# Kernel optimization log

Measured on AMD Instinct MI355X. Metric: run time of the kernel, lower is better.

The kernel has to match this reference:

```python
import jax, jax.numpy as jnp
import numpy as np

B, C, H, W = 8, 512, 64, 64
DEPTH, HEADS = 4, 8


def setup_inputs() -> dict:
    key = jax.random.key(0)
    ks = jax.random.split(key, 7)
    s = 0.02
    return {
        "x": jax.random.normal(ks[0], (B, C, H, W), jnp.float32),
        # axial positional embeddings, emb dim at index 1: (1,C,H,1) and (1,C,1,W)
        "pos_h": jax.random.normal(ks[1], (C, H), jnp.float32) * s,
        "pos_w": jax.random.normal(ks[2], (C, W), jnp.float32) * s,
        # per layer, per axis (0=height, 1=width): q, kv, out projections
        "wq": jax.random.normal(ks[3], (DEPTH, 2, C, C), jnp.float32) * s,
        "wkv": jax.random.normal(ks[4], (DEPTH, 2, C, 2 * C), jnp.float32) * s,
        "wo": jax.random.normal(ks[5], (DEPTH, 2, C, C), jnp.float32) * s,
        "wo_b": jax.random.normal(ks[6], (DEPTH, 2, C), jnp.float32) * s,
    }


def _attn_last_axis(x, wq, wkv, wo, wo_b, heads):
    """Self-attention along the second-to-last axis. x: (..., L, C)."""
    lead = x.shape[:-2]
    L, Cd = x.shape[-2], x.shape[-1]
    e = Cd // heads
    q = x @ wq                       # (..., L, C)
    k, v = jnp.split(x @ wkv, 2, axis=-1)
    sh = lead + (L, heads, e)
    q, k, v = q.reshape(sh), k.reshape(sh), v.reshape(sh)
    dots = jnp.einsum('...ihe,...jhe->...hij', q, k) * (e ** -0.5)
    attn = jax.nn.softmax(dots, axis=-1)
    out = jnp.einsum('...hij,...jhe->...ihe', attn, v).reshape(lead + (L, heads * e))
    return out @ wo + wo_b


def reference(x, pos_h, pos_w, wq, wkv, wo, wo_b):
    # positional embedding: x + (1,C,H,1) + (1,C,1,W)
    x = x + pos_h[None, :, :, None] + pos_w[None, :, None, :]
    y = jnp.transpose(x, (0, 2, 3, 1))  # (B,H,W,C) channels-last working layout
    for l in range(DEPTH):
        # height-axis attention: (B,W,H,C), attend along H
        yh = jnp.transpose(y, (0, 2, 1, 3))
        oh = _attn_last_axis(yh, wq[l, 0], wkv[l, 0], wo[l, 0], wo_b[l, 0], HEADS)
        oh = jnp.transpose(oh, (0, 2, 1, 3))
        # width-axis attention: attend along W
        ow = _attn_last_axis(y, wq[l, 1], wkv[l, 1], wo[l, 1], wo_b[l, 1], HEADS)
        y = oh + ow  # sum_axial_out=True, no residual
    return jnp.transpose(y, (0, 3, 1, 2))  # back to (B,C,H,W)
```

## Files before the change

### kernel.cpp

```cpp
#include <hip/hip_runtime.h>
#include <stdint.h>


typedef __attribute__((ext_vector_type(8))) short bf16x8;
typedef __attribute__((ext_vector_type(4))) float f32x4;
typedef unsigned short u16;
typedef unsigned int u32;

#define MFMA16(a, b, c) __builtin_amdgcn_mfma_f32_16x16x32_bf16((a), (b), (c), 0, 0, 0)

__device__ __forceinline__ float b2f(u16 h) {
    u32 u = ((u32)h) << 16;
    float f;
    __builtin_memcpy(&f, &u, 4);
    return f;
}
__device__ __forceinline__ u16 f2b(float f) {
    u32 u;
    __builtin_memcpy(&u, &f, 4);
    u32 r = (u + 0x7fffu + ((u >> 16) & 1u)) >> 16;
    return (u16)r;
}

#define GLD_LDS16(g, l)                                                        \
    __builtin_amdgcn_global_load_lds(                                          \
        (const __attribute__((address_space(1))) void*)(g),                    \
        (__attribute__((address_space(3))) void*)(l), 16, 0, 0)

__global__ __launch_bounds__(256) void embed_kernel(
    const float* __restrict__ x, const float* __restrict__ ph,
    const float* __restrict__ pw, u16* __restrict__ y)
{
    __shared__ float tile[64][65];
    const int c0 = blockIdx.x * 64, h = blockIdx.y, b = blockIdx.z;
    const int t = threadIdx.x;
#pragma unroll
    for (int i = 0; i < 4; ++i) {
        int cl = (t >> 4) + i * 16;
        int w4 = (t & 15) * 4;
        const float* src = x + (((size_t)(b * 512 + c0 + cl)) * 64 + h) * 64 + w4;
        float4 v = *(const float4*)src;
        float p = ph[(c0 + cl) * 64 + h];
        tile[cl][w4 + 0] = v.x + p + pw[(c0 + cl) * 64 + w4 + 0];
        tile[cl][w4 + 1] = v.y + p + pw[(c0 + cl) * 64 + w4 + 1];
        tile[cl][w4 + 2] = v.z + p + pw[(c0 + cl) * 64 + w4 + 2];
        tile[cl][w4 + 3] = v.w + p + pw[(c0 + cl) * 64 + w4 + 3];
    }
    __syncthreads();
    const int wl = t >> 2, cb = (t & 3) * 16;
    bf16x8 o0, o1;
#pragma unroll
    for (int j = 0; j < 8; ++j) o0[j] = (short)f2b(tile[cb + j][wl]);
#pragma unroll
    for (int j = 0; j < 8; ++j) o1[j] = (short)f2b(tile[cb + 8 + j][wl]);
    u16* dst = y + (((size_t)(b * 64 + h) * 64 + wl) * 512 + c0 + cb);
    *(bf16x8*)dst = o0;
    *(bf16x8*)(dst + 8) = o1;
}

__global__ __launch_bounds__(256) void wtrans_kernel(
    const float* __restrict__ wq, const float* __restrict__ wkv,
    const float* __restrict__ wo, u16* __restrict__ wT)
{
    const int mid = blockIdx.z;
    const int l = mid / 6, rest = mid % 6, axis = rest / 3, which = rest % 3;
    const size_t la = (size_t)(l * 2 + axis);
    const float* src;
    int N;
    size_t doff;
    if (which == 0)      { src = wq  + la * 512 * 512;  N = 512;  doff = la * (2048 * 512); }
    else if (which == 1) { src = wkv + la * 512 * 1024; N = 1024; doff = la * (2048 * 512) + 512 * 512; }
    else                 { src = wo  + la * 512 * 512;  N = 512;  doff = la * (2048 * 512) + 512 * 512 + 1024 * 512; }
    const int n0 = blockIdx.y * 64;
    if (n0 >= N) return;
    const int k0 = blockIdx.x * 64;
    __shared__ float tile[64][65];
    const int t = threadIdx.x;
#pragma unroll
    for (int i = 0; i < 4; ++i) {
        int kl = (t >> 4) + i * 16;
        int n4 = (t & 15) * 4;
        float4 v = *(const float4*)(src + (size_t)(k0 + kl) * N + n0 + n4);
        tile[kl][n4 + 0] = v.x; tile[kl][n4 + 1] = v.y;
        tile[kl][n4 + 2] = v.z; tile[kl][n4 + 3] = v.w;
    }
    __syncthreads();
    const int nl = t >> 2, kb = (t & 3) * 16;
    bf16x8 o0, o1;
#pragma unroll
    for (int j = 0; j < 8; ++j) o0[j] = (short)f2b(tile[kb + j][nl]);
#pragma unroll
    for (int j = 0; j < 8; ++j) o1[j] = (short)f2b(tile[kb + 8 + j][nl]);
    u16* dst = wT + doff + (size_t)(n0 + nl) * 512 + k0 + kb;
    *(bf16x8*)dst = o0;
    *(bf16x8*)(dst + 8) = o1;
}

template <int MODE, int PERM>
__global__ __launch_bounds__(512, 2) void gemm256(
    const u16* __restrict__ A, int lda,
    const u16* __restrict__ Bt,
    const float* __restrict__ bias,
    u16* C, int ldc)
{
    __shared__ u16 As[2][256 * 64];
    __shared__ u16 Bs[2][256 * 64];
    const int tid = threadIdx.x, lane = tid & 63, wid = tid >> 6;
    const int wm = wid >> 2, wn = wid & 3;
    int lin = blockIdx.x + gridDim.x * blockIdx.y;
    int cpx = (gridDim.x * gridDim.y) >> 3;
    int id = (lin & 7) * cpx + (lin >> 3);
    const int n0 = (id % gridDim.x) * 256;
    const int m0 = (id / gridDim.x) * 256;
    const int rl = lane >> 3, cp = lane & 7, l16 = lane & 15, g = lane >> 4;
    const int kgrp = g << 3;

    f32x4 acc[4][8] = {};

#define STAGE(b, ks)                                                           \
    {                                                                          \
        _Pragma("unroll")                                                      \
        for (int j = 0; j < 4; ++j) {                                          \
            int grp = wid + 8 * j;                                             \
            int row = grp * 8 + rl;                                            \
            const u16* s = A + (size_t)(m0 + row) * lda + (ks) + (cp ^ (row & 7)) * 8; \
            GLD_LDS16(s, As[b] + grp * 512);                                   \
        }                                                                      \
        _Pragma("unroll")                                                      \
        for (int j = 0; j < 4; ++j) {                                          \
            int grp = wid + 8 * j;                                             \
            int row = grp * 8 + rl;                                            \
            const u16* s = Bt + (size_t)(n0 + row) * 512 + (ks) + (cp ^ (row & 7)) * 8; \
            GLD_LDS16(s, Bs[b] + grp * 512);                                   \
        }                                                                      \
    }

#define FRAG(base, row, kk)                                                    \
    (*(const bf16x8*)((const char*)(base) + (row) * 128 +                      \
                      (((kk) * 64 + g * 16) ^ (((row) & 7) << 4))))

    STAGE(0, 0);

    for (int t = 0; t < 8; ++t) {
        const int cb = t & 1;
        if (t < 7) STAGE(cb ^ 1, (t + 1) * 64);
        __builtin_amdgcn_sched_barrier(0);
        if (t < 7) { asm volatile("s_waitcnt vmcnt(8)" ::: "memory"); }
        else       { asm volatile("s_waitcnt vmcnt(0)" ::: "memory"); }
        __builtin_amdgcn_s_barrier();
        __builtin_amdgcn_sched_barrier(0);

        const u16* cA = As[cb];
        const u16* cB = Bs[cb];
        bf16x8 bl[2][2], bh[2][2], af[4][2];

#pragma unroll
        for (int nf = 0; nf < 2; ++nf)
#pragma unroll
            for (int kk = 0; kk < 2; ++kk)
                bl[nf][kk] = FRAG(cB, wn * 64 + nf * 16 + l16, kk);
#pragma unroll
        for (int mf = 0; mf < 4; ++mf)
#pragma unroll
            for (int kk = 0; kk < 2; ++kk)
                af[mf][kk] = FRAG(cA, wm * 128 + mf * 16 + l16, kk);
        __builtin_amdgcn_s_setprio(1);
#pragma unroll
        for (int kk = 0; kk < 2; ++kk)
#pragma unroll
            for (int nf = 0; nf < 2; ++nf)
#pragma unroll
                for (int mf = 0; mf < 4; ++mf)
                    acc[nf][mf] = MFMA16(bl[nf][kk], af[mf][kk], acc[nf][mf]);
        __builtin_amdgcn_s_setprio(0);

#pragma unroll
        for (int nf = 0; nf < 2; ++nf)
#pragma unroll
            for (int kk = 0; kk < 2; ++kk)
                bh[nf][kk] = FRAG(cB, wn * 64 + 32 + nf * 16 + l16, kk);
        __builtin_amdgcn_s_setprio(1);
#pragma unroll
        for (int kk = 0; kk < 2; ++kk)
#pragma unroll
            for (int nf = 0; nf < 2; ++nf)
#pragma unroll
                for (int mf = 0; mf < 4; ++mf)
                    acc[2 + nf][mf] = MFMA16(bh[nf][kk], af[mf][kk], acc[2 + nf][mf]);
        __builtin_amdgcn_s_setprio(0);

#pragma unroll
        for (int mf = 0; mf < 4; ++mf)
#pragma unroll
            for (int kk = 0; kk < 2; ++kk)
                af[mf][kk] = FRAG(cA, wm * 128 + 64 + mf * 16 + l16, kk);
        __builtin_amdgcn_s_setprio(1);
#pragma unroll
        for (int kk = 0; kk < 2; ++kk)
#pragma unroll
            for (int nf = 0; nf < 2; ++nf)
#pragma unroll
                for (int mf = 0; mf < 4; ++mf)
                    acc[2 + nf][4 + mf] = MFMA16(bh[nf][kk], af[mf][kk], acc[2 + nf][4 + mf]);
        __builtin_amdgcn_s_setprio(0);

        __builtin_amdgcn_s_setprio(1);
#pragma unroll
        for (int kk = 0; kk < 2; ++kk)
#pragma unroll
            for (int nf = 0; nf < 2; ++nf)
#pragma unroll
                for (int mf = 0; mf < 4; ++mf)
                    acc[nf][4 + mf] = MFMA16(bl[nf][kk], af[mf][kk], acc[nf][4 + mf]);
        __builtin_amdgcn_s_setprio(0);

        __builtin_amdgcn_sched_barrier(0);
        __builtin_amdgcn_s_barrier();
        __builtin_amdgcn_sched_barrier(0);
    }

    float bv[4][4];
    if (MODE >= 1) {
#pragma unroll
        for (int nf = 0; nf < 4; ++nf) {
            float4 b4 = *(const float4*)(bias + n0 + wn * 64 + nf * 16 + g * 4);
            bv[nf][0] = b4.x; bv[nf][1] = b4.y; bv[nf][2] = b4.z; bv[nf][3] = b4.w;
        }
    }
#pragma unroll
    for (int mf = 0; mf < 8; ++mf) {
        const int m = m0 + wm * 128 + mf * 16 + l16;
        const int mp = PERM ? ((m & ~4095) | ((m & 63) << 6) | ((m >> 6) & 63)) : m;
        u16* crow = C + (size_t)mp * ldc;
#pragma unroll
        for (int nf = 0; nf < 4; ++nf) {
            const int n = n0 + wn * 64 + nf * 16 + g * 4;
            u16* cptr = crow + n;
            float v0 = acc[nf][mf][0], v1 = acc[nf][mf][1];
            float v2 = acc[nf][mf][2], v3 = acc[nf][mf][3];
            if (MODE >= 1) { v0 += bv[nf][0]; v1 += bv[nf][1]; v2 += bv[nf][2]; v3 += bv[nf][3]; }
            if (MODE == 2) {
                ushort4 o = *(const ushort4*)cptr;
                v0 += b2f(o.x); v1 += b2f(o.y); v2 += b2f(o.z); v3 += b2f(o.w);
            }
            uint2 pk;
            pk.x = (u32)f2b(v0) | ((u32)f2b(v1) << 16);
            pk.y = (u32)f2b(v2) | ((u32)f2b(v3) << 16);
            *(uint2*)cptr = pk;
        }
    }
#undef STAGE
#undef FRAG
}

__global__ __launch_bounds__(256) void attn_kernel(u16* QKV)
{
    __shared__ u16 sm[4][2][64 * 64];
    const int tid = threadIdx.x, lane = tid & 63, wv = tid >> 6;
    const int unit = blockIdx.x * 4 + wv;
    const int base = (unit >> 3) * 64;
    const int hoff = (unit & 7) * 64;
    const int l16 = lane & 15, g = lane >> 4;
    const int kgrp = g << 3;
    const int rl = lane >> 3, cp = lane & 7;
    u16* Kl = (u16*)sm[wv][0];
    u16* Vt = (u16*)sm[wv][1];

#pragma unroll
    for (int i = 0; i < 8; ++i) {
        int row = i * 8 + rl;
        int clog = cp ^ (row & 7);
        const u16* src = QKV + (size_t)(base + row) * 1536 + 512 + hoff + clog * 8;
        GLD_LDS16(src, Kl + i * 8 * 64);
    }
    bf16x8 q[4][2];
#pragma unroll
    for (int i_f = 0; i_f < 4; ++i_f)
#pragma unroll
        for (int k2 = 0; k2 < 2; ++k2)
            q[i_f][k2] = *(const bf16x8*)(QKV + (size_t)(base + i_f * 16 + l16) * 1536
                                          + hoff + k2 * 32 + kgrp);
    bf16x8 vvr[8];
#pragma unroll
    for (int i = 0; i < 8; ++i)
        vvr[i] = *(const bf16x8*)(QKV + (size_t)(base + i * 8 + rl) * 1536
                                  + 1024 + hoff + cp * 8);

    asm volatile("s_waitcnt vmcnt(0)" ::: "memory");
    __builtin_amdgcn_sched_barrier(0);

    f32x4 st[4][4] = {};
#pragma unroll
    for (int k2 = 0; k2 < 2; ++k2) {
        bf16x8 kf[4];
        const int kb = (k2 * 32 + kgrp) * 2;
#pragma unroll
        for (int j_f = 0; j_f < 4; ++j_f) {
            int row = j_f * 16 + l16;
            kf[j_f] = *(const bf16x8*)((const char*)Kl + row * 128 + (kb ^ ((row & 7) << 4)));
        }
#pragma unroll
        for (int i_f = 0; i_f < 4; ++i_f)
#pragma unroll
            for (int j_f = 0; j_f < 4; ++j_f)
                st[i_f][j_f] = MFMA16(kf[j_f], q[i_f][k2], st[i_f][j_f]);
    }

#pragma unroll
    for (int i = 0; i < 8; ++i) {
        int j2 = i * 16 + rl * 2;
#pragma unroll
        for (int t = 0; t < 8; ++t) {
            int e = cp * 8 + t;
            int addr = e * 128 + (j2 ^ (((t ^ cp) & 7) << 4));
            *(u16*)((char*)Vt + addr) = (u16)vvr[i][t];
        }
    }

#pragma unroll
    for (int i_f = 0; i_f < 4; ++i_f) {
        const int irow = i_f * 16 + l16;
        float ev[4][4];
        float mx = -1e30f;
#pragma unroll
        for (int j_f = 0; j_f < 4; ++j_f)
#pragma unroll
            for (int r = 0; r < 4; ++r) {
                float v = st[i_f][j_f][r] * 0.125f;
                ev[j_f][r] = v;
                mx = fmaxf(mx, v);
            }
        mx = fmaxf(mx, __shfl_xor(mx, 16, 64));
        mx = fmaxf(mx, __shfl_xor(mx, 32, 64));
        float sum = 0.f;
#pragma unroll
        for (int j_f = 0; j_f < 4; ++j_f)
#pragma unroll
            for (int r = 0; r < 4; ++r) {
                float e = __expf(ev[j_f][r] - mx);
                ev[j_f][r] = e;
                sum += e;
            }
        sum += __shfl_xor(sum, 16, 64);
        sum += __shfl_xor(sum, 32, 64);
        float inv = __builtin_amdgcn_rcpf(sum);
#pragma unroll
        for (int j_f = 0; j_f < 4; ++j_f) {
            uint2 pk;
            pk.x = (u32)f2b(ev[j_f][0] * inv) | ((u32)f2b(ev[j_f][1] * inv) << 16);
            pk.y = (u32)f2b(ev[j_f][2] * inv) | ((u32)f2b(ev[j_f][3] * inv) << 16);
            int addr = irow * 128 + ((j_f * 32 + g * 8) ^ ((irow & 7) << 4));
            *(uint2*)((char*)Kl + addr) = pk;
        }
    }

    f32x4 of[4][4] = {};
#pragma unroll
    for (int k2 = 0; k2 < 2; ++k2) {
        bf16x8 vf[4], pf[4];
        const int kb = (k2 * 32 + kgrp) * 2;
#pragma unroll
        for (int e_f = 0; e_f < 4; ++e_f) {
            int row = e_f * 16 + l16;
            int sw = ((row & 7) ^ ((row >> 3) & 7)) << 4;
            vf[e_f] = *(const bf16x8*)((const char*)Vt + row * 128 + (kb ^ sw));
        }
#pragma unroll
        for (int i_f = 0; i_f < 4; ++i_f) {
            int row = i_f * 16 + l16;
            pf[i_f] = *(const bf16x8*)((const char*)Kl + row * 128 + (kb ^ ((row & 7) << 4)));
        }
#pragma unroll
        for (int e_f = 0; e_f < 4; ++e_f)
#pragma unroll
            for (int i_f = 0; i_f < 4; ++i_f)
                of[e_f][i_f] = MFMA16(vf[e_f], pf[i_f], of[e_f][i_f]);
    }

#pragma unroll
    for (int i_f = 0; i_f < 4; ++i_f) {
        const int i = i_f * 16 + l16;
        u16* orow = QKV + (size_t)(base + i) * 1536 + hoff + g * 4;
#pragma unroll
        for (int e_f = 0; e_f < 4; ++e_f) {
            uint2 pk;
            pk.x = (u32)f2b(of[e_f][i_f][0]) | ((u32)f2b(of[e_f][i_f][1]) << 16);
            pk.y = (u32)f2b(of[e_f][i_f][2]) | ((u32)f2b(of[e_f][i_f][3]) << 16);
            *(uint2*)(orow + e_f * 16) = pk;
        }
    }
}

__global__ __launch_bounds__(256) void untrans_kernel(
    const u16* __restrict__ y, float* __restrict__ out)
{
    __shared__ float tile[64][65];
    const int c0 = blockIdx.x * 64, h = blockIdx.y, b = blockIdx.z;
    const int t = threadIdx.x;
    {
        const int wl = t >> 2, cb = (t & 3) * 16;
        const u16* src = y + (((size_t)(b * 64 + h) * 64 + wl) * 512 + c0 + cb);
        bf16x8 v0 = *(const bf16x8*)src;
        bf16x8 v1 = *(const bf16x8*)(src + 8);
#pragma unroll
        for (int j = 0; j < 8; ++j) tile[wl][cb + j] = b2f((u16)v0[j]);
#pragma unroll
        for (int j = 0; j < 8; ++j) tile[wl][cb + 8 + j] = b2f((u16)v1[j]);
    }
    __syncthreads();
    const int cl = t >> 2, w16 = (t & 3) * 16;
    float* dst = out + (((size_t)(b * 512 + c0 + cl)) * 64 + h) * 64 + w16;
#pragma unroll
    for (int j = 0; j < 4; ++j) {
        float4 v;
        v.x = tile[w16 + j * 4 + 0][cl];
        v.y = tile[w16 + j * 4 + 1][cl];
        v.z = tile[w16 + j * 4 + 2][cl];
        v.w = tile[w16 + j * 4 + 3][cl];
        *(float4*)(dst + j * 4) = v;
    }
}

extern "C" void kernel_launch(void* const* d_in, const int* in_sizes, int n_in,
                              void* d_out, int out_size, void* d_ws, size_t ws_size,
                              hipStream_t stream)
{
    (void)in_sizes; (void)n_in; (void)out_size; (void)ws_size;
    const float* x   = (const float*)d_in[0];
    const float* ph  = (const float*)d_in[1];
    const float* pw  = (const float*)d_in[2];
    const float* wq  = (const float*)d_in[3];
    const float* wkv = (const float*)d_in[4];
    const float* wo  = (const float*)d_in[5];
    const float* wob = (const float*)d_in[6];

    char* ws = (char*)d_ws;
    u16* yA  = (u16*)(ws);
    u16* yB  = (u16*)(ws + 33554432);
    u16* QKV = (u16*)(ws + 67108864);
    u16* wT  = (u16*)(ws + 167772160);
    float* out = (float*)d_out;

    embed_kernel<<<dim3(8, 64, 8), 256, 0, stream>>>(x, ph, pw, yA);
    wtrans_kernel<<<dim3(8, 16, 24), 256, 0, stream>>>(wq, wkv, wo, wT);

    u16* yin = yA;
    u16* yout = yB;
    for (int l = 0; l < 4; ++l) {
        for (int axis = 0; axis < 2; ++axis) {
            const u16* wTla = wT + (size_t)(l * 2 + axis) * 2048 * 512;
            const float* bias = wob + (size_t)(l * 2 + axis) * 512;
            const u16* woT = wTla + 512 * 512 + 1024 * 512;
            if (axis == 0)
                gemm256<0, 1><<<dim3(6, 128), 512, 0, stream>>>(yin, 512, wTla, nullptr, QKV, 1536);
            else
                gemm256<0, 0><<<dim3(6, 128), 512, 0, stream>>>(yin, 512, wTla, nullptr, QKV, 1536);
            attn_kernel<<<dim3(1024), 256, 0, stream>>>(QKV);
            if (axis == 0)
                gemm256<1, 1><<<dim3(2, 128), 512, 0, stream>>>(QKV, 1536, woT, bias, yout, 512);
            else
                gemm256<2, 0><<<dim3(2, 128), 512, 0, stream>>>(QKV, 1536, woT, bias, yout, 512);
        }
        u16* tmp = yin; yin = yout; yout = tmp;
    }
    untrans_kernel<<<dim3(8, 64, 8), 256, 0, stream>>>(yin, out);
}
```

Baseline: 1.076 ms.

## Fuse QKV projection into per-head attention kernel, drop QKV buffer

Replaces the separate QKV GEMM and attention kernel with one kernel. In it, each wave computes its head's Q, K and V projections for one 64-length sequence straight from global memory, then runs the softmax attention. Fragments are moved between MFMA layouts through a small per-wave LDS scratch. This removes the write and re-read of the large QKV intermediate and one launch per axis. The permuted output addressing also becomes strided input addressing. The cost is that each activation row is re-read by all 8 heads and weights are re-read per wave without LDS tiling, so the kernel leans heavily on L2 and cache reuse.

```diff
diff --git a/kernel.cpp b/kernel.cpp
--- a/kernel.cpp
+++ b/kernel.cpp
@@ -8,6 +8,7 @@
 typedef unsigned int u32;
 
 #define MFMA16(a, b, c) __builtin_amdgcn_mfma_f32_16x16x32_bf16((a), (b), (c), 0, 0, 0)
+#define SBAR() __builtin_amdgcn_sched_barrier(0)
 
 __device__ __forceinline__ float b2f(u16 h) {
     u32 u = ((u32)h) << 16;
@@ -20,6 +21,12 @@
     __builtin_memcpy(&u, &f, 4);
     u32 r = (u + 0x7fffu + ((u >> 16) & 1u)) >> 16;
     return (u16)r;
+}
+__device__ __forceinline__ uint2 pack4(const f32x4& v) {
+    uint2 pk;
+    pk.x = (u32)f2b(v[0]) | ((u32)f2b(v[1]) << 16);
+    pk.y = (u32)f2b(v[2]) | ((u32)f2b(v[3]) << 16);
+    return pk;
 }
 
 #define GLD_LDS16(g, l)                                                        \
@@ -96,7 +103,198 @@
     *(bf16x8*)(dst + 8) = o1;
 }
 
-template <int MODE, int PERM>
+template <int AXIS>
+__global__ __launch_bounds__(256, 4) void qkv_attn(
+    const u16* __restrict__ y,
+    const u16* __restrict__ wTla,
+    u16* __restrict__ O)
+{
+    __shared__ u16 scrb[4][1024];
+    const int tid = threadIdx.x, lane = tid & 63, wv = tid >> 6;
+    const int unit = blockIdx.x * 4 + wv;
+    const int seq = unit >> 3, head = unit & 7;
+    const int l16 = lane & 15, g = lane >> 4;
+    const size_t rowbase = ((size_t)(seq >> 6) << 12) +
+                           (AXIS == 0 ? (size_t)(seq & 63) : ((size_t)(seq & 63) << 6));
+    const int rowstr = (AXIS == 0) ? 64 : 1;
+    u16* scr = (u16*)scrb[wv];
+
+    const int hoff = head * 64;
+    const u16* wq_ = wTla + (size_t)hoff * 512;
+    const u16* wk_ = wTla + (size_t)(512 + hoff) * 512;
+    const u16* wv_ = wTla + (size_t)(1024 + hoff) * 512;
+
+#define YG(r, t) (*(const bf16x8*)(y + (rowbase + (size_t)(r) * rowstr) * 512 + (t) * 32 + g * 8))
+#define SW16(bo, val) *(uint2*)((char*)scr + l16 * 128 + ((bo) ^ ((l16 & 7) << 4))) = (val)
+#define SF16(k2) (*(const bf16x8*)((const char*)scr + l16 * 128 + \
+                    (((k2) * 64 + g * 16) ^ ((l16 & 7) << 4))))
+
+    f32x4 acc[4][4];
+    bf16x8 kf[4][2], qf[4][2];
+
+#pragma unroll
+    for (int ef = 0; ef < 4; ++ef)
+#pragma unroll
+        for (int jf = 0; jf < 4; ++jf) acc[ef][jf] = f32x4{0.f, 0.f, 0.f, 0.f};
+#pragma unroll
+    for (int t = 0; t < 16; ++t) {
+        bf16x8 yf[4], wf[4];
+#pragma unroll
+        for (int f = 0; f < 4; ++f) {
+            int row = f * 16 + l16;
+            yf[f] = YG(row, t);
+            wf[f] = *(const bf16x8*)(wk_ + (size_t)row * 512 + t * 32 + g * 8);
+        }
+#pragma unroll
+        for (int ef = 0; ef < 4; ++ef)
+#pragma unroll
+            for (int jf = 0; jf < 4; ++jf)
+                acc[ef][jf] = MFMA16(wf[ef], yf[jf], acc[ef][jf]);
+    }
+#pragma unroll
+    for (int jf = 0; jf < 4; ++jf) {
+#pragma unroll
+        for (int ef = 0; ef < 4; ++ef)
+            SW16((ef * 16 + g * 4) * 2, pack4(acc[ef][jf]));
+        SBAR();
+        kf[jf][0] = SF16(0);
+        kf[jf][1] = SF16(1);
+        SBAR();
+    }
+
+#pragma unroll
+    for (int ef = 0; ef < 4; ++ef)
+#pragma unroll
+        for (int jf = 0; jf < 4; ++jf) acc[ef][jf] = f32x4{0.f, 0.f, 0.f, 0.f};
+#pragma unroll
+    for (int t = 0; t < 16; ++t) {
+        bf16x8 yf[4], wf[4];
+#pragma unroll
+        for (int f = 0; f < 4; ++f) {
+            int row = f * 16 + l16;
+            yf[f] = YG(row, t);
+            wf[f] = *(const bf16x8*)(wq_ + (size_t)row * 512 + t * 32 + g * 8);
+        }
+#pragma unroll
+        for (int ef = 0; ef < 4; ++ef)
+#pragma unroll
+            for (int jf = 0; jf < 4; ++jf)
+                acc[ef][jf] = MFMA16(wf[ef], yf[jf], acc[ef][jf]);
+    }
+#pragma unroll
+    for (int jf = 0; jf < 4; ++jf) {
+#pragma unroll
+        for (int ef = 0; ef < 4; ++ef)
+            SW16((ef * 16 + g * 4) * 2, pack4(acc[ef][jf]));
+        SBAR();
+        qf[jf][0] = SF16(0);
+        qf[jf][1] = SF16(1);
+        SBAR();
+    }
+
+    f32x4 st[4][4] = {};
+#pragma unroll
+    for (int k2 = 0; k2 < 2; ++k2)
+#pragma unroll
+        for (int i_f = 0; i_f < 4; ++i_f)
+#pragma unroll
+            for (int j_f = 0; j_f < 4; ++j_f)
+                st[i_f][j_f] = MFMA16(kf[j_f][k2], qf[i_f][k2], st[i_f][j_f]);
+
+    bf16x8 pf[4][2];
+#pragma unroll
+    for (int i_f = 0; i_f < 4; ++i_f) {
+        float ev[4][4];
+        float mx = -1e30f;
+#pragma unroll
+        for (int j_f = 0; j_f < 4; ++j_f)
+#pragma unroll
+            for (int r = 0; r < 4; ++r) {
+                float v = st[i_f][j_f][r] * 0.125f;
+                ev[j_f][r] = v;
+                mx = fmaxf(mx, v);
+            }
+        mx = fmaxf(mx, __shfl_xor(mx, 16, 64));
+        mx = fmaxf(mx, __shfl_xor(mx, 32, 64));
+        float sum = 0.f;
+#pragma unroll
+        for (int j_f = 0; j_f < 4; ++j_f)
+#pragma unroll
+            for (int r = 0; r < 4; ++r) {
+                float e = __expf(ev[j_f][r] - mx);
+                ev[j_f][r] = e;
+                sum += e;
+            }
+        sum += __shfl_xor(sum, 16, 64);
+        sum += __shfl_xor(sum, 32, 64);
+        float inv = __builtin_amdgcn_rcpf(sum);
+#pragma unroll
+        for (int j_f = 0; j_f < 4; ++j_f) {
+            uint2 pk;
+            pk.x = (u32)f2b(ev[j_f][0] * inv) | ((u32)f2b(ev[j_f][1] * inv) << 16);
+            pk.y = (u32)f2b(ev[j_f][2] * inv) | ((u32)f2b(ev[j_f][3] * inv) << 16);
+            SW16(j_f * 32 + g * 8, pk);
+        }
+        SBAR();
+        pf[i_f][0] = SF16(0);
+        pf[i_f][1] = SF16(1);
+        SBAR();
+    }
+
+#pragma unroll
+    for (int jf = 0; jf < 4; ++jf)
+#pragma unroll
+        for (int ef = 0; ef < 4; ++ef) acc[jf][ef] = f32x4{0.f, 0.f, 0.f, 0.f};
+#pragma unroll
+    for (int t = 0; t < 16; ++t) {
+        bf16x8 yf[4], wf[4];
+#pragma unroll
+        for (int f = 0; f < 4; ++f) {
+            int row = f * 16 + l16;
+            yf[f] = YG(row, t);
+            wf[f] = *(const bf16x8*)(wv_ + (size_t)row * 512 + t * 32 + g * 8);
+        }
+#pragma unroll
+        for (int jf = 0; jf < 4; ++jf)
+#pragma unroll
+            for (int ef = 0; ef < 4; ++ef)
+                acc[jf][ef] = MFMA16(yf[jf], wf[ef], acc[jf][ef]);
+    }
+    bf16x8 vtf[4][2];
+#pragma unroll
+    for (int ef = 0; ef < 4; ++ef) {
+#pragma unroll
+        for (int jf = 0; jf < 4; ++jf)
+            SW16((jf * 16 + g * 4) * 2, pack4(acc[jf][ef]));
+        SBAR();
+        vtf[ef][0] = SF16(0);
+        vtf[ef][1] = SF16(1);
+        SBAR();
+    }
+
+    f32x4 of[4][4] = {};
+#pragma unroll
+    for (int k2 = 0; k2 < 2; ++k2)
+#pragma unroll
+        for (int ef = 0; ef < 4; ++ef)
+#pragma unroll
+            for (int i_f = 0; i_f < 4; ++i_f)
+                of[ef][i_f] = MFMA16(vtf[ef][k2], pf[i_f][k2], of[ef][i_f]);
+
+#pragma unroll
+    for (int i_f = 0; i_f < 4; ++i_f) {
+        const int i = i_f * 16 + l16;
+        u16* orow = O + (rowbase + (size_t)i * rowstr) * 512 + hoff + g * 4;
+#pragma unroll
+        for (int ef = 0; ef < 4; ++ef)
+            *(uint2*)(orow + ef * 16) = pack4(of[ef][i_f]);
+    }
+#undef YG
+#undef SW16
+#undef SF16
+}
+
+template <int MODE>
 __global__ __launch_bounds__(512, 2) void gemm256(
     const u16* __restrict__ A, int lda,
     const u16* __restrict__ Bt,
@@ -113,7 +311,6 @@
     const int n0 = (id % gridDim.x) * 256;
     const int m0 = (id / gridDim.x) * 256;
     const int rl = lane >> 3, cp = lane & 7, l16 = lane & 15, g = lane >> 4;
-    const int kgrp = g << 3;
 
     f32x4 acc[4][8] = {};
 
@@ -220,25 +417,22 @@
     }
 
     float bv[4][4];
-    if (MODE >= 1) {
-#pragma unroll
-        for (int nf = 0; nf < 4; ++nf) {
-            float4 b4 = *(const float4*)(bias + n0 + wn * 64 + nf * 16 + g * 4);
-            bv[nf][0] = b4.x; bv[nf][1] = b4.y; bv[nf][2] = b4.z; bv[nf][3] = b4.w;
-        }
+#pragma unroll
+    for (int nf = 0; nf < 4; ++nf) {
+        float4 b4 = *(const float4*)(bias + n0 + wn * 64 + nf * 16 + g * 4);
+        bv[nf][0] = b4.x; bv[nf][1] = b4.y; bv[nf][2] = b4.z; bv[nf][3] = b4.w;
     }
 #pragma unroll
     for (int mf = 0; mf < 8; ++mf) {
         const int m = m0 + wm * 128 + mf * 16 + l16;
-        const int mp = PERM ? ((m & ~4095) | ((m & 63) << 6) | ((m >> 6) & 63)) : m;
-        u16* crow = C + (size_t)mp * ldc;
+        u16* crow = C + (size_t)m * ldc;
 #pragma unroll
         for (int nf = 0; nf < 4; ++nf) {
             const int n = n0 + wn * 64 + nf * 16 + g * 4;
             u16* cptr = crow + n;
             float v0 = acc[nf][mf][0], v1 = acc[nf][mf][1];
             float v2 = acc[nf][mf][2], v3 = acc[nf][mf][3];
-            if (MODE >= 1) { v0 += bv[nf][0]; v1 += bv[nf][1]; v2 += bv[nf][2]; v3 += bv[nf][3]; }
+            v0 += bv[nf][0]; v1 += bv[nf][1]; v2 += bv[nf][2]; v3 += bv[nf][3];
             if (MODE == 2) {
                 ushort4 o = *(const ushort4*)cptr;
                 v0 += b2f(o.x); v1 += b2f(o.y); v2 += b2f(o.z); v3 += b2f(o.w);
@@ -251,144 +445,6 @@
     }
 #undef STAGE
 #undef FRAG
-}
-
-__global__ __launch_bounds__(256) void attn_kernel(u16* QKV)
-{
-    __shared__ u16 sm[4][2][64 * 64];
-    const int tid = threadIdx.x, lane = tid & 63, wv = tid >> 6;
-    const int unit = blockIdx.x * 4 + wv;
-    const int base = (unit >> 3) * 64;
-    const int hoff = (unit & 7) * 64;
-    const int l16 = lane & 15, g = lane >> 4;
-    const int kgrp = g << 3;
-    const int rl = lane >> 3, cp = lane & 7;
-    u16* Kl = (u16*)sm[wv][0];
-    u16* Vt = (u16*)sm[wv][1];
-
-#pragma unroll
-    for (int i = 0; i < 8; ++i) {
-        int row = i * 8 + rl;
-        int clog = cp ^ (row & 7);
-        const u16* src = QKV + (size_t)(base + row) * 1536 + 512 + hoff + clog * 8;
-        GLD_LDS16(src, Kl + i * 8 * 64);
-    }
-    bf16x8 q[4][2];
-#pragma unroll
-    for (int i_f = 0; i_f < 4; ++i_f)
-#pragma unroll
-        for (int k2 = 0; k2 < 2; ++k2)
-            q[i_f][k2] = *(const bf16x8*)(QKV + (size_t)(base + i_f * 16 + l16) * 1536
-                                          + hoff + k2 * 32 + kgrp);
-    bf16x8 vvr[8];
-#pragma unroll
-    for (int i = 0; i < 8; ++i)
-        vvr[i] = *(const bf16x8*)(QKV + (size_t)(base + i * 8 + rl) * 1536
-                                  + 1024 + hoff + cp * 8);
-
-    asm volatile("s_waitcnt vmcnt(0)" ::: "memory");
-    __builtin_amdgcn_sched_barrier(0);
-
-    f32x4 st[4][4] = {};
-#pragma unroll
-    for (int k2 = 0; k2 < 2; ++k2) {
-        bf16x8 kf[4];
-        const int kb = (k2 * 32 + kgrp) * 2;
-#pragma unroll
-        for (int j_f = 0; j_f < 4; ++j_f) {
-            int row = j_f * 16 + l16;
-            kf[j_f] = *(const bf16x8*)((const char*)Kl + row * 128 + (kb ^ ((row & 7) << 4)));
-        }
-#pragma unroll
-        for (int i_f = 0; i_f < 4; ++i_f)
-#pragma unroll
-            for (int j_f = 0; j_f < 4; ++j_f)
-                st[i_f][j_f] = MFMA16(kf[j_f], q[i_f][k2], st[i_f][j_f]);
-    }
-
-#pragma unroll
-    for (int i = 0; i < 8; ++i) {
-        int j2 = i * 16 + rl * 2;
-#pragma unroll
-        for (int t = 0; t < 8; ++t) {
-            int e = cp * 8 + t;
-            int addr = e * 128 + (j2 ^ (((t ^ cp) & 7) << 4));
-            *(u16*)((char*)Vt + addr) = (u16)vvr[i][t];
-        }
-    }
-
-#pragma unroll
-    for (int i_f = 0; i_f < 4; ++i_f) {
-        const int irow = i_f * 16 + l16;
-        float ev[4][4];
-        float mx = -1e30f;
-#pragma unroll
-        for (int j_f = 0; j_f < 4; ++j_f)
-#pragma unroll
-            for (int r = 0; r < 4; ++r) {
-                float v = st[i_f][j_f][r] * 0.125f;
-                ev[j_f][r] = v;
-                mx = fmaxf(mx, v);
-            }
-        mx = fmaxf(mx, __shfl_xor(mx, 16, 64));
-        mx = fmaxf(mx, __shfl_xor(mx, 32, 64));
-        float sum = 0.f;
-#pragma unroll
-        for (int j_f = 0; j_f < 4; ++j_f)
-#pragma unroll
-            for (int r = 0; r < 4; ++r) {
-                float e = __expf(ev[j_f][r] - mx);
-                ev[j_f][r] = e;
-                sum += e;
-            }
-        sum += __shfl_xor(sum, 16, 64);
-        sum += __shfl_xor(sum, 32, 64);
-        float inv = __builtin_amdgcn_rcpf(sum);
-#pragma unroll
-        for (int j_f = 0; j_f < 4; ++j_f) {
-            uint2 pk;
-            pk.x = (u32)f2b(ev[j_f][0] * inv) | ((u32)f2b(ev[j_f][1] * inv) << 16);
-            pk.y = (u32)f2b(ev[j_f][2] * inv) | ((u32)f2b(ev[j_f][3] * inv) << 16);
-            int addr = irow * 128 + ((j_f * 32 + g * 8) ^ ((irow & 7) << 4));
-            *(uint2*)((char*)Kl + addr) = pk;
-        }
-    }
-
-    f32x4 of[4][4] = {};
-#pragma unroll
-    for (int k2 = 0; k2 < 2; ++k2) {
-        bf16x8 vf[4], pf[4];
-        const int kb = (k2 * 32 + kgrp) * 2;
-#pragma unroll
-        for (int e_f = 0; e_f < 4; ++e_f) {
-            int row = e_f * 16 + l16;
-            int sw = ((row & 7) ^ ((row >> 3) & 7)) << 4;
-            vf[e_f] = *(const bf16x8*)((const char*)Vt + row * 128 + (kb ^ sw));
-        }
-#pragma unroll
-        for (int i_f = 0; i_f < 4; ++i_f) {
-            int row = i_f * 16 + l16;
-            pf[i_f] = *(const bf16x8*)((const char*)Kl + row * 128 + (kb ^ ((row & 7) << 4)));
-        }
-#pragma unroll
-        for (int e_f = 0; e_f < 4; ++e_f)
-#pragma unroll
-            for (int i_f = 0; i_f < 4; ++i_f)
-                of[e_f][i_f] = MFMA16(vf[e_f], pf[i_f], of[e_f][i_f]);
-    }
-
-#pragma unroll
-    for (int i_f = 0; i_f < 4; ++i_f) {
-        const int i = i_f * 16 + l16;
-        u16* orow = QKV + (size_t)(base + i) * 1536 + hoff + g * 4;
-#pragma unroll
-        for (int e_f = 0; e_f < 4; ++e_f) {
-            uint2 pk;
-            pk.x = (u32)f2b(of[e_f][i_f][0]) | ((u32)f2b(of[e_f][i_f][1]) << 16);
-            pk.y = (u32)f2b(of[e_f][i_f][2]) | ((u32)f2b(of[e_f][i_f][3]) << 16);
-            *(uint2*)(orow + e_f * 16) = pk;
-        }
-    }
 }
 
 __global__ __launch_bounds__(256) void untrans_kernel(
@@ -435,10 +491,10 @@
     const float* wob = (const float*)d_in[6];
 
     char* ws = (char*)d_ws;
-    u16* yA  = (u16*)(ws);
-    u16* yB  = (u16*)(ws + 33554432);
-    u16* QKV = (u16*)(ws + 67108864);
-    u16* wT  = (u16*)(ws + 167772160);
+    u16* yA = (u16*)(ws);
+    u16* yB = (u16*)(ws + 33554432);
+    u16* O  = (u16*)(ws + 67108864);
+    u16* wT = (u16*)(ws + 100663296);
     float* out = (float*)d_out;
 
     embed_kernel<<<dim3(8, 64, 8), 256, 0, stream>>>(x, ph, pw, yA);
@@ -451,15 +507,13 @@
             const u16* wTla = wT + (size_t)(l * 2 + axis) * 2048 * 512;
             const float* bias = wob + (size_t)(l * 2 + axis) * 512;
             const u16* woT = wTla + 512 * 512 + 1024 * 512;
-            if (axis == 0)
-                gemm256<0, 1><<<dim3(6, 128), 512, 0, stream>>>(yin, 512, wTla, nullptr, QKV, 1536);
-            else
-                gemm256<0, 0><<<dim3(6, 128), 512, 0, stream>>>(yin, 512, wTla, nullptr, QKV, 1536);
-            attn_kernel<<<dim3(1024), 256, 0, stream>>>(QKV);
-            if (axis == 0)
-                gemm256<1, 1><<<dim3(2, 128), 512, 0, stream>>>(QKV, 1536, woT, bias, yout, 512);
-            else
-                gemm256<2, 0><<<dim3(2, 128), 512, 0, stream>>>(QKV, 1536, woT, bias, yout, 512);
+            if (axis == 0) {
+                qkv_attn<0><<<dim3(1024), 256, 0, stream>>>(yin, wTla, O);
+                gemm256<1><<<dim3(2, 128), 512, 0, stream>>>(O, 512, woT, bias, yout, 512);
+            } else {
+                qkv_attn<1><<<dim3(1024), 256, 0, stream>>>(yin, wTla, O);
+                gemm256<2><<<dim3(2, 128), 512, 0, stream>>>(O, 512, woT, bias, yout, 512);
+            }
         }
         u16* tmp = yin; yin = yout; yout = tmp;
     }
```

Measured after the change: 1.836 ms. 70.6% more time.

## Interleave next-tile global-to-LDS loads across MFMA phases in GEMM

Applied to the files above, without the earlier changes.

The GEMM main loop used to issue all eight global-to-LDS loads for the next K tile at the start of each iteration. It now splits them into four pairs, one issued after each MFMA phase, with an extra workgroup barrier between phases and a vmcnt(2) wait. The goal is to spread memory traffic across the compute phases so it overlaps better with MFMA work. In exchange it adds three barriers per iteration, which may cost some synchronisation time. The attention kernel change only renames a variable.

```diff
diff --git a/kernel.cpp b/kernel.cpp
--- a/kernel.cpp
+++ b/kernel.cpp
@@ -113,47 +113,38 @@
     const int n0 = (id % gridDim.x) * 256;
     const int m0 = (id / gridDim.x) * 256;
     const int rl = lane >> 3, cp = lane & 7, l16 = lane & 15, g = lane >> 4;
-    const int kgrp = g << 3;
 
     f32x4 acc[4][8] = {};
 
-#define STAGE(b, ks)                                                           \
+#define STAGE1(b, ks, j)                                                       \
     {                                                                          \
-        _Pragma("unroll")                                                      \
-        for (int j = 0; j < 4; ++j) {                                          \
-            int grp = wid + 8 * j;                                             \
-            int row = grp * 8 + rl;                                            \
-            const u16* s = A + (size_t)(m0 + row) * lda + (ks) + (cp ^ (row & 7)) * 8; \
-            GLD_LDS16(s, As[b] + grp * 512);                                   \
-        }                                                                      \
-        _Pragma("unroll")                                                      \
-        for (int j = 0; j < 4; ++j) {                                          \
-            int grp = wid + 8 * j;                                             \
-            int row = grp * 8 + rl;                                            \
-            const u16* s = Bt + (size_t)(n0 + row) * 512 + (ks) + (cp ^ (row & 7)) * 8; \
-            GLD_LDS16(s, Bs[b] + grp * 512);                                   \
-        }                                                                      \
+        int grp = wid + 8 * (j);                                               \
+        int row = grp * 8 + rl;                                                \
+        const u16* sA = A + (size_t)(m0 + row) * lda + (ks) + (cp ^ (row & 7)) * 8; \
+        GLD_LDS16(sA, As[b] + grp * 512);                                      \
+        const u16* sB = Bt + (size_t)(n0 + row) * 512 + (ks) + (cp ^ (row & 7)) * 8; \
+        GLD_LDS16(sB, Bs[b] + grp * 512);                                      \
     }
 
 #define FRAG(base, row, kk)                                                    \
     (*(const bf16x8*)((const char*)(base) + (row) * 128 +                      \
                       (((kk) * 64 + g * 16) ^ (((row) & 7) << 4))))
 
-    STAGE(0, 0);
+#pragma unroll
+    for (int j = 0; j < 4; ++j) STAGE1(0, 0, j);
 
     for (int t = 0; t < 8; ++t) {
         const int cb = t & 1;
-        if (t < 7) STAGE(cb ^ 1, (t + 1) * 64);
+        const u16* cA = As[cb];
+        const u16* cB = Bs[cb];
+        bf16x8 bl[2][2], bh[2][2], af[4][2];
+
+        if (t < 7) STAGE1(cb ^ 1, (t + 1) * 64, 0);
         __builtin_amdgcn_sched_barrier(0);
-        if (t < 7) { asm volatile("s_waitcnt vmcnt(8)" ::: "memory"); }
+        if (t < 7) { asm volatile("s_waitcnt vmcnt(2)" ::: "memory"); }
         else       { asm volatile("s_waitcnt vmcnt(0)" ::: "memory"); }
         __builtin_amdgcn_s_barrier();
         __builtin_amdgcn_sched_barrier(0);
-
-        const u16* cA = As[cb];
-        const u16* cB = Bs[cb];
-        bf16x8 bl[2][2], bh[2][2], af[4][2];
-
 #pragma unroll
         for (int nf = 0; nf < 2; ++nf)
 #pragma unroll
@@ -173,7 +164,9 @@
                 for (int mf = 0; mf < 4; ++mf)
                     acc[nf][mf] = MFMA16(bl[nf][kk], af[mf][kk], acc[nf][mf]);
         __builtin_amdgcn_s_setprio(0);
-
+        __builtin_amdgcn_s_barrier();
+
+        if (t < 7) STAGE1(cb ^ 1, (t + 1) * 64, 1);
 #pragma unroll
         for (int nf = 0; nf < 2; ++nf)
 #pragma unroll
@@ -188,7 +181,9 @@
                 for (int mf = 0; mf < 4; ++mf)
                     acc[2 + nf][mf] = MFMA16(bh[nf][kk], af[mf][kk], acc[2 + nf][mf]);
         __builtin_amdgcn_s_setprio(0);
-
+        __builtin_amdgcn_s_barrier();
+
+        if (t < 7) STAGE1(cb ^ 1, (t + 1) * 64, 2);
 #pragma unroll
         for (int mf = 0; mf < 4; ++mf)
 #pragma unroll
@@ -203,7 +198,9 @@
                 for (int mf = 0; mf < 4; ++mf)
                     acc[2 + nf][4 + mf] = MFMA16(bh[nf][kk], af[mf][kk], acc[2 + nf][4 + mf]);
         __builtin_amdgcn_s_setprio(0);
-
+        __builtin_amdgcn_s_barrier();
+
+        if (t < 7) STAGE1(cb ^ 1, (t + 1) * 64, 3);
         __builtin_amdgcn_s_setprio(1);
 #pragma unroll
         for (int kk = 0; kk < 2; ++kk)
@@ -213,7 +210,6 @@
                 for (int mf = 0; mf < 4; ++mf)
                     acc[nf][4 + mf] = MFMA16(bl[nf][kk], af[mf][kk], acc[nf][4 + mf]);
         __builtin_amdgcn_s_setprio(0);
-
         __builtin_amdgcn_sched_barrier(0);
         __builtin_amdgcn_s_barrier();
         __builtin_amdgcn_sched_barrier(0);
@@ -249,7 +245,7 @@
             *(uint2*)cptr = pk;
         }
     }
-#undef STAGE
+#undef STAGE1
 #undef FRAG
 }
 
@@ -357,7 +353,7 @@
     f32x4 of[4][4] = {};
 #pragma unroll
     for (int k2 = 0; k2 < 2; ++k2) {
-        bf16x8 vf[4], pf[4];
+        bf16x8 vf[4], pfr[4];
         const int kb = (k2 * 32 + kgrp) * 2;
 #pragma unroll
         for (int e_f = 0; e_f < 4; ++e_f) {
@@ -368,13 +364,13 @@
 #pragma unroll
         for (int i_f = 0; i_f < 4; ++i_f) {
             int row = i_f * 16 + l16;
-            pf[i_f] = *(const bf16x8*)((const char*)Kl + row * 128 + (kb ^ ((row & 7) << 4)));
+            pfr[i_f] = *(const bf16x8*)((const char*)Kl + row * 128 + (kb ^ ((row & 7) << 4)));
         }
 #pragma unroll
         for (int e_f = 0; e_f < 4; ++e_f)
 #pragma unroll
             for (int i_f = 0; i_f < 4; ++i_f)
-                of[e_f][i_f] = MFMA16(vf[e_f], pf[i_f], of[e_f][i_f]);
+                of[e_f][i_f] = MFMA16(vf[e_f], pfr[i_f], of[e_f][i_f]);
     }
 
 #pragma unroll
```

Result: slower. 1.198 ms (+11.3%).
